# Kernel optimization log

Hardware: AMD Instinct MI355X
Metric: run time of the kernel (lower is better)

The kernel has to match this reference:

```python
import jax, jax.numpy as jnp
import numpy as np

B, N, D, H = 8, 2048, 128, 4
DH = D // H
EPS_LN = 1e-5


def setup_inputs() -> dict:
    key = jax.random.key(0)
    ks = jax.random.split(key, 9)
    x = jax.random.normal(ks[0], (B, N, D), dtype=jnp.float32)
    u = jax.random.uniform(ks[1], (N, N), dtype=jnp.float32)
    adj = jnp.where(u > 0.5, u, 0.0)
    adj = adj.at[jnp.arange(N), jnp.arange(N)].set(1.0)
    W = jax.random.normal(ks[2], (D, D), dtype=jnp.float32) * (1.0 / np.sqrt(D))
    a_src = jax.random.normal(ks[3], (H, DH), dtype=jnp.float32) * 0.02
    a_dst = jax.random.normal(ks[4], (H, DH), dtype=jnp.float32) * 0.02
    Wo = jax.random.normal(ks[5], (D, D), dtype=jnp.float32) * (1.0 / np.sqrt(D))
    bo = jnp.zeros((D,), dtype=jnp.float32)
    gamma = jnp.ones((D,), dtype=jnp.float32)
    beta = jnp.zeros((D,), dtype=jnp.float32)
    return {"x": x, "adj_static": adj, "W": W, "a_src": a_src, "a_dst": a_dst,
            "Wo": Wo, "bo": bo, "gamma": gamma, "beta": beta}


def reference(x, adj_static, W, a_src, a_dst, Wo, bo, gamma, beta):
    # h: (B, H, N, DH)
    h = (x @ W.T).reshape(B, N, H, DH).transpose(0, 2, 1, 3)
    src = jnp.einsum('bhnd,hd->bhn', h, a_src)  # (B, H, N)
    dst = jnp.einsum('bhnd,hd->bhn', h, a_dst)  # (B, H, N)
    e = jax.nn.leaky_relu(src[..., :, None] + dst[..., None, :], 0.2)  # (B,H,N,N)
    logA = jnp.log(jnp.clip(adj_static, 1e-8))[None, None]
    mask = (adj_static > 0)[None, None]
    e = jnp.where(mask, e + logA, -jnp.inf)
    attn = jax.nn.softmax(e, axis=-1)  # dropout is identity in eval mode
    out = attn @ h  # (B, H, N, DH)
    out = out.transpose(0, 2, 1, 3).reshape(B, N, D)
    out = out @ Wo.T + bo
    y = x + out
    mu = jnp.mean(y, axis=-1, keepdims=True)
    var = jnp.mean(jnp.square(y - mu), axis=-1, keepdims=True)
    return (y - mu) * jax.lax.rsqrt(var + EPS_LN) * gamma + beta
```

## Files before the change

### kernel.cpp

```cpp
#include <hip/hip_runtime.h>

typedef short bf16x8 __attribute__((ext_vector_type(8)));
typedef float f32x4  __attribute__((ext_vector_type(4)));
typedef float f32x2  __attribute__((ext_vector_type(2)));
typedef int   i32x4  __attribute__((ext_vector_type(4)));
typedef unsigned int u32x2 __attribute__((ext_vector_type(2)));

#define DEV static __device__ __forceinline__
#define LOG2E 1.4426950408889634f

DEV float bfu_to_f(unsigned short s) { return __builtin_bit_cast(float, (unsigned int)s << 16); }
DEV unsigned short f_to_bf(float f) {
  unsigned int u = __builtin_bit_cast(unsigned int, f);
  u += 0x7fffu + ((u >> 16) & 1u);
  return (unsigned short)(u >> 16);
}
DEV unsigned int pack_bf_rne(float lo, float hi) {
  return (unsigned int)f_to_bf(lo) | ((unsigned int)f_to_bf(hi) << 16);
}
DEV float nexp2(float x) {
#if __has_builtin(__builtin_amdgcn_exp2f)
  return __builtin_amdgcn_exp2f(x);
#else
  return exp2f(x);
#endif
}
template<bool HI> DEV unsigned int pk_fp8(float a, float b, unsigned int old) {
  return __builtin_amdgcn_cvt_pk_fp8_f32(a, b, old, HI);
}
template<int W> DEV f32x2 upk_fp8(unsigned int w) {
  auto r = __builtin_amdgcn_cvt_pk_f32_fp8(w, W);
  f32x2 o; o[0] = r[0]; o[1] = r[1]; return o;
}

DEV bool detect_f32(const void* adj) { return ((const float*)adj)[0] == 1.0f; }

template<bool F32> DEV float ldS(const void* p, size_t i) {
  if constexpr (F32) return ((const float*)p)[i];
  else               return bfu_to_f(((const unsigned short*)p)[i]);
}
template<bool F32> DEV void ld8f(const void* p, size_t i, float* o) {
  if constexpr (F32) {
    const float* f = (const float*)p + i;
    f32x4 a = *(const f32x4*)f, b = *(const f32x4*)(f + 4);
    o[0]=a[0]; o[1]=a[1]; o[2]=a[2]; o[3]=a[3];
    o[4]=b[0]; o[5]=b[1]; o[6]=b[2]; o[7]=b[3];
  } else {
    i32x4 w = *(const i32x4*)((const unsigned short*)p + i);
#pragma unroll
    for (int k = 0; k < 4; ++k) {
      unsigned int u = (unsigned int)w[k];
      o[2*k]   = __builtin_bit_cast(float, u << 16);
      o[2*k+1] = __builtin_bit_cast(float, u & 0xffff0000u);
    }
  }
}
template<bool F32> DEV bf16x8 ldfrag(const void* p, size_t i) {
  if constexpr (F32) {
    float o[8]; ld8f<true>(p, i, o);
    union { bf16x8 v; unsigned short u[8]; } r;
#pragma unroll
    for (int k = 0; k < 8; ++k) r.u[k] = f_to_bf(o[k]);
    return r.v;
  } else {
    return __builtin_bit_cast(bf16x8, *(const i32x4*)((const unsigned short*)p + i));
  }
}

__global__ __launch_bounds__(256) void k_prep(const void* __restrict__ adj,
                                              unsigned char* __restrict__ adjf) {
  const size_t i0 = ((size_t)blockIdx.x * 256 + threadIdx.x) * 8;
  u32x2 o;
  if (detect_f32(adj)) {
    const float* a = (const float*)adj + i0;
    f32x4 v0 = *(const f32x4*)a, v1 = *(const f32x4*)(a + 4);
    o[0] = pk_fp8<true>(v0[2], v0[3], pk_fp8<false>(v0[0], v0[1], 0u));
    o[1] = pk_fp8<true>(v1[2], v1[3], pk_fp8<false>(v1[0], v1[1], 0u));
  } else {
    i32x4 w = *(const i32x4*)((const unsigned short*)adj + i0);
    float f[8];
#pragma unroll
    for (int k = 0; k < 4; ++k) {
      unsigned int u = (unsigned int)w[k];
      f[2*k]   = __builtin_bit_cast(float, u << 16);
      f[2*k+1] = __builtin_bit_cast(float, u & 0xffff0000u);
    }
    o[0] = pk_fp8<true>(f[2], f[3], pk_fp8<false>(f[0], f[1], 0u));
    o[1] = pk_fp8<true>(f[6], f[7], pk_fp8<false>(f[4], f[5], 0u));
  }
  *(u32x2*)(adjf + i0) = o;
}

template<bool F32> DEV void k_h_body(const void* __restrict__ x, const void* __restrict__ W,
                                     unsigned char* __restrict__ hT,
                                     unsigned short (&t_s)[16][136]) {
  const int tid = threadIdx.x, lane = tid & 63, wave = tid >> 6;
  const int nt = blockIdx.x >> 3, ct = blockIdx.x & 7;
  const int m = lane & 15, q = lane >> 4;
  bf16x8 wf[4];
#pragma unroll
  for (int k = 0; k < 4; ++k)
    wf[k] = ldfrag<F32>(W, (size_t)(ct * 16 + m) * 128 + q * 8 + k * 32);
#pragma unroll
  for (int s = 0; s < 2; ++s) {
    const int nsub = wave * 2 + s;
    const size_t xr = (size_t)(nt * 128 + nsub * 16 + m) * 128 + q * 8;
    f32x4 acc = {0.f, 0.f, 0.f, 0.f};
#pragma unroll
    for (int k = 0; k < 4; ++k)
      acc = __builtin_amdgcn_mfma_f32_16x16x32_bf16(ldfrag<F32>(x, xr + k * 32), wf[k],
                                                    acc, 0, 0, 0);
    u32x2 w2; w2[0] = pack_bf_rne(acc[0], acc[1]); w2[1] = pack_bf_rne(acc[2], acc[3]);
    *(u32x2*)&t_s[m][nsub * 16 + q * 4] = w2;
  }
  __syncthreads();
  const int row = tid >> 4, c8 = tid & 15;
  const int chg = ct * 16 + row, hh = chg >> 5, dloc = chg & 31;
  const int ng = nt * 128 + c8 * 8, b = ng >> 11, nl = ng & 2047;
  i32x4 v = *(const i32x4*)&t_s[row][c8 * 8];
  float f[8];
#pragma unroll
  for (int k = 0; k < 4; ++k) {
    unsigned int u = (unsigned int)v[k];
    f[2*k]   = __builtin_bit_cast(float, u << 16);
    f[2*k+1] = __builtin_bit_cast(float, u & 0xffff0000u);
  }
  u32x2 o;
  o[0] = pk_fp8<true>(f[2], f[3], pk_fp8<false>(f[0], f[1], 0u));
  o[1] = pk_fp8<true>(f[6], f[7], pk_fp8<false>(f[4], f[5], 0u));
  *(u32x2*)(hT + ((size_t)((b * 4 + hh) * 32 + dloc)) * 2048 + nl) = o;
}
__global__ __launch_bounds__(256) void k_h(const void* x, const void* W,
                                           unsigned char* hT, const void* adj) {
  __shared__ __align__(16) unsigned short t_s[16][136];
  if (detect_f32(adj)) k_h_body<true>(x, W, hT, t_s); else k_h_body<false>(x, W, hT, t_s);
}

template<bool F32> DEV void k_sd_body(const unsigned char* __restrict__ hT,
                                      const void* __restrict__ a_src, const void* __restrict__ a_dst,
                                      float* __restrict__ rv, float* __restrict__ Fv,
                                      float* __restrict__ Hv) {
  const int t = blockIdx.x * 256 + threadIdx.x;
  const int n = t & 2047, bh = t >> 11, hh = bh & 3;
  const unsigned char* col = hT + (size_t)bh * 32 * 2048 + n;
  float s = 0.f, d = 0.f;
#pragma unroll
  for (int dd = 0; dd < 32; ++dd) {
    const float v = __builtin_amdgcn_cvt_f32_fp8((int)col[(size_t)dd * 2048], 0);
    s += v * ldS<F32>(a_src, hh * 32 + dd);
    d += v * ldS<F32>(a_dst, hh * 32 + dd);
  }
  rv[t] = nexp2(-0.8f * LOG2E * s);
  Fv[t] = nexp2(LOG2E * d);
  Hv[t] = nexp2(0.2f * LOG2E * d);
}
__global__ __launch_bounds__(256) void k_sd(const unsigned char* hT, const void* a_src,
                                            const void* a_dst, float* rv, float* Fv,
                                            float* Hv, const void* adj) {
  if (detect_f32(adj)) k_sd_body<true>(hT, a_src, a_dst, rv, Fv, Hv);
  else                 k_sd_body<false>(hT, a_src, a_dst, rv, Fv, Hv);
}

struct SmemAttn {
  unsigned char adj[2][64][144];
  unsigned char vt[2][32][144];
  float F[2][128];
  float H[2][128];
};

__global__ __launch_bounds__(512, 4) void k_attn(const unsigned char* __restrict__ adjf,
                                                 const unsigned char* __restrict__ hT,
                                                 const float* __restrict__ rv,
                                                 const float* __restrict__ Fv,
                                                 const float* __restrict__ Hv,
                                                 unsigned short* __restrict__ ao) {
  __shared__ __align__(16) SmemAttn sm;
  const int tid = threadIdx.x, lane = tid & 63, wave = tid >> 6;
  const int bh = blockIdx.x & 31, i64 = blockIdx.x >> 5;
  const int b = bh >> 2, hh = bh & 3;
  const int m = lane & 15, q = lane >> 4;
  const int i0 = i64 * 64;
  const int itile = wave >> 1, jh = wave & 1;
  const int il = itile * 16 + m;

  const int arow = tid >> 3, acol = (tid & 7) * 16;
  const int vd = tid >> 4, vcol = (tid & 15) * 8;
  const int scls = tid & 15;
  const bool dstg = scls < 2;
  const int dj = (tid >> 4) * 4;

  const unsigned char* ap = adjf + (size_t)(i0 + arow) * 2048 + acol;
  const unsigned char* vp = hT + ((size_t)bh * 32 + vd) * 2048 + vcol;
  const float* dp = (scls == 0 ? Fv : Hv) + (size_t)bh * 2048 + dj;
  float* dbase = (scls == 0 ? &sm.F[0][dj] : &sm.H[0][dj]);

  i32x4 ar; u32x2 vr; f32x4 dr;

  ar = *(const i32x4*)ap;
  vr = *(const u32x2*)vp;
  if (dstg) dr = *(const f32x4*)dp;
  *(i32x4*)&sm.adj[0][arow][acol] = ar;
  *(u32x2*)&sm.vt[0][vd][vcol] = vr;
  if (dstg) *(f32x4*)dbase = dr;
  __syncthreads();

  const float Ri = rv[bh * 2048 + i0 + il];
  const f32x2 Ri2 = {Ri, Ri};
  f32x4 acc0 = {0.f,0.f,0.f,0.f}, acc1 = {0.f,0.f,0.f,0.f};
  f32x4 acc2 = {0.f,0.f,0.f,0.f};
  const long Aones = 0x3838383838383838L;

  for (int c = 0; c < 16; ++c) {
    const int cb = c & 1;
    const bool pf = (c < 15);
    if (pf) {
      const int j1 = (c + 1) * 128;
      ar = *(const i32x4*)(ap + j1);
      vr = *(const u32x2*)(vp + j1);
      if (dstg) dr = *(const f32x4*)(dp + j1);
    }
#pragma unroll
    for (int jc = 0; jc < 2; ++jc) {
      const int jq = jh * 64 + jc * 32 + q * 8;
      u32x2 aw = *(const u32x2*)&sm.adj[cb][il][jq];
      f32x4 Fa = *(const f32x4*)&sm.F[cb][jq];
      f32x4 Fb = *(const f32x4*)&sm.F[cb][jq + 4];
      f32x4 Ha = *(const f32x4*)&sm.H[cb][jq];
      f32x4 Hb = *(const f32x4*)&sm.H[cb][jq + 4];
      long A0 = *(const long*)&sm.vt[cb][m][jq];
      long A1 = *(const long*)&sm.vt[cb][16 + m][jq];
      f32x2 av0 = upk_fp8<0>(aw[0]), av1 = upk_fp8<1>(aw[0]);
      f32x2 av2 = upk_fp8<0>(aw[1]), av3 = upk_fp8<1>(aw[1]);
      f32x2 f0 = {Fa[0],Fa[1]}, f1 = {Fa[2],Fa[3]};
      f32x2 f2 = {Fb[0],Fb[1]}, f3 = {Fb[2],Fb[3]};
      f32x2 h0 = {Ha[0],Ha[1]}, h1 = {Ha[2],Ha[3]};
      f32x2 h2 = {Hb[0],Hb[1]}, h3 = {Hb[2],Hb[3]};
      f32x2 w0 = __builtin_elementwise_max(f0, Ri2 * h0);
      f32x2 w1 = __builtin_elementwise_max(f1, Ri2 * h1);
      f32x2 w2 = __builtin_elementwise_max(f2, Ri2 * h2);
      f32x2 w3 = __builtin_elementwise_max(f3, Ri2 * h3);
      f32x2 pv0 = av0 * w0, pv1 = av1 * w1, pv2 = av2 * w2, pv3 = av3 * w3;
      u32x2 bp;
      bp[0] = pk_fp8<true>(pv1[0], pv1[1], pk_fp8<false>(pv0[0], pv0[1], 0u));
      bp[1] = pk_fp8<true>(pv3[0], pv3[1], pk_fp8<false>(pv2[0], pv2[1], 0u));
      const long B = __builtin_bit_cast(long, bp);
      acc0 = __builtin_amdgcn_mfma_f32_16x16x32_fp8_fp8(A0, B, acc0, 0, 0, 0);
      acc1 = __builtin_amdgcn_mfma_f32_16x16x32_fp8_fp8(A1, B, acc1, 0, 0, 0);
      acc2 = __builtin_amdgcn_mfma_f32_16x16x32_fp8_fp8(Aones, B, acc2, 0, 0, 0);
    }
    if (pf) {
      const int nb = cb ^ 1;
      *(i32x4*)&sm.adj[nb][arow][acol] = ar;
      *(u32x2*)&sm.vt[nb][vd][vcol] = vr;
      if (dstg) *(f32x4*)(dbase + nb * 128) = dr;
    }
    __syncthreads();
  }

  float* red = (float*)&sm;
  const int ridx = (itile * 64 + lane) * 12;
  if (jh == 1) {
    *(f32x4*)&red[ridx]     = acc0;
    *(f32x4*)&red[ridx + 4] = acc1;
    red[ridx + 8] = acc2[0];
  }
  __syncthreads();
  if (jh == 0) {
    acc0 += *(const f32x4*)&red[ridx];
    acc1 += *(const f32x4*)&red[ridx + 4];
    const float den = acc2[0] + red[ridx + 8];
    const float inv = 1.f / fmaxf(den, 1e-20f);
    unsigned short* op = ao + ((size_t)(b * 2048) + i0 + il) * 128 + hh * 32 + q * 4;
    u32x2 w0, w1;
    w0[0] = pack_bf_rne(acc0[0] * inv, acc0[1] * inv);
    w0[1] = pack_bf_rne(acc0[2] * inv, acc0[3] * inv);
    w1[0] = pack_bf_rne(acc1[0] * inv, acc1[1] * inv);
    w1[1] = pack_bf_rne(acc1[2] * inv, acc1[3] * inv);
    *(u32x2*)op        = w0;
    *(u32x2*)(op + 16) = w1;
  }
}

template<bool F32> DEV void k_out_body(const unsigned short* __restrict__ ao,
                                       const void* __restrict__ Wo, const void* __restrict__ bo,
                                       const void* __restrict__ x, const void* __restrict__ gamma,
                                       const void* __restrict__ beta, void* __restrict__ out,
                                       float (&y_s)[16][132]) {
  const int tid = threadIdx.x, lane = tid & 63, wave = tid >> 6;
  const int m = lane & 15, q = lane >> 4;
  const int rbase = blockIdx.x * 16;
  bf16x8 af[4];
#pragma unroll
  for (int k = 0; k < 4; ++k)
    af[k] = ldfrag<false>(ao, ((size_t)(rbase + m)) * 128 + q * 8 + k * 32);
  f32x4 acc[2] = {{0.f,0.f,0.f,0.f},{0.f,0.f,0.f,0.f}};
#pragma unroll
  for (int ct = 0; ct < 2; ++ct) {
    const size_t wrow = (size_t)(wave * 32 + ct * 16 + m) * 128 + q * 8;
#pragma unroll
    for (int k = 0; k < 4; ++k)
      acc[ct] = __builtin_amdgcn_mfma_f32_16x16x32_bf16(af[k], ldfrag<F32>(Wo, wrow + k * 32),
                                                        acc[ct], 0, 0, 0);
  }
#pragma unroll
  for (int ct = 0; ct < 2; ++ct) {
    const int c = wave * 32 + ct * 16 + m;
    const float bov = ldS<F32>(bo, c);
#pragma unroll
    for (int r = 0; r < 4; ++r) {
      const int row = q * 4 + r;
      y_s[row][c] = acc[ct][r] + bov + ldS<F32>(x, (size_t)(rbase + row) * 128 + c);
    }
  }
  __syncthreads();
  const int r = tid >> 4, c16 = tid & 15;
  float vals[8], sum = 0.f, sq = 0.f;
#pragma unroll
  for (int k = 0; k < 8; ++k) {
    const float v = y_s[r][c16 * 8 + k];
    vals[k] = v; sum += v; sq += v * v;
  }
#pragma unroll
  for (int msk = 1; msk < 16; msk <<= 1) {
    sum += __shfl_xor(sum, msk, 16);
    sq  += __shfl_xor(sq,  msk, 16);
  }
  const float mu  = sum * (1.f / 128.f);
  const float var = fmaxf(sq * (1.f / 128.f) - mu * mu, 0.f);
  const float rstd = rsqrtf(var + 1e-5f);
  float o[8];
#pragma unroll
  for (int k = 0; k < 8; ++k) {
    const int c = c16 * 8 + k;
    o[k] = (vals[k] - mu) * rstd * ldS<F32>(gamma, c) + ldS<F32>(beta, c);
  }
  const size_t obase = (size_t)(rbase + r) * 128 + c16 * 8;
  if constexpr (F32) {
    float* op = (float*)out + obase;
    f32x4 w0 = {o[0],o[1],o[2],o[3]}, w1 = {o[4],o[5],o[6],o[7]};
    *(f32x4*)op = w0; *(f32x4*)(op + 4) = w1;
  } else {
    union { unsigned short u[8]; i32x4 v; } ob;
#pragma unroll
    for (int k = 0; k < 8; ++k) ob.u[k] = f_to_bf(o[k]);
    *(i32x4*)((unsigned short*)out + obase) = ob.v;
  }
}
__global__ __launch_bounds__(256) void k_out(const unsigned short* ao, const void* Wo,
                                             const void* bo, const void* x, const void* gamma,
                                             const void* beta, void* out, const void* adj) {
  __shared__ __align__(16) float y_s[16][132];
  if (detect_f32(adj)) k_out_body<true>(ao, Wo, bo, x, gamma, beta, out, y_s);
  else                 k_out_body<false>(ao, Wo, bo, x, gamma, beta, out, y_s);
}

extern "C" void kernel_launch(void* const* d_in, const int* in_sizes, int n_in,
                              void* d_out, int out_size, void* d_ws, size_t ws_size,
                              hipStream_t stream) {
  const void* x     = d_in[0];
  const void* adj   = d_in[1];
  const void* W     = d_in[2];
  const void* a_src = d_in[3];
  const void* a_dst = d_in[4];
  const void* Wo    = d_in[5];
  const void* bo    = d_in[6];
  const void* gamma = d_in[7];
  const void* beta  = d_in[8];

  char* ws = (char*)d_ws;
  unsigned char*  hT_ws  = (unsigned char*)ws;
  unsigned short* ao_ws  = (unsigned short*)(ws + 2097152);
  float*          rv_ws  = (float*)(ws + 6291456);
  float*          Fv_ws  = (float*)(ws + 6553600);
  float*          Hv_ws  = (float*)(ws + 6815744);
  unsigned char*  adjf   = (unsigned char*)(ws + 7077888);

  k_prep<<<2048, 256, 0, stream>>>(adj, adjf);
  k_h   <<<1024, 256, 0, stream>>>(x, W, hT_ws, adj);
  k_sd  <<<256,  256, 0, stream>>>(hT_ws, a_src, a_dst, rv_ws, Fv_ws, Hv_ws, adj);
  k_attn<<<1024, 512, 0, stream>>>(adjf, hT_ws, rv_ws, Fv_ws, Hv_ws, ao_ws);
  k_out <<<1024, 256, 0, stream>>>(ao_ws, Wo, bo, x, gamma, beta, d_out, adj);
}
```

Measured before the change: 148.9 us.

## Drop LDS staging in attention; load operands directly into registers with bf16-packed F/H

The attention kernel no longer stages adjacency, value and F/H tiles through double-buffered shared memory with per-chunk barriers. Each wave now loads its own fragments straight from global memory into a two-deep register prefetch ring. F and H are stored as one packed bf16 pair per element, halving that traffic, and blocks shrink to 256 threads covering 32 rows, with twice as many blocks. This removes LDS round-trips and barriers, but operands shared across waves are now fetched redundantly from global/L2, and F/H lose precision to bf16.

```diff
diff --git a/kernel.cpp b/kernel.cpp
--- a/kernel.cpp
+++ b/kernel.cpp
@@ -18,6 +18,8 @@
 DEV unsigned int pack_bf_rne(float lo, float hi) {
   return (unsigned int)f_to_bf(lo) | ((unsigned int)f_to_bf(hi) << 16);
 }
+DEV float fplo(int u) { return __builtin_bit_cast(float, (unsigned int)u << 16); }
+DEV float fphi(int u) { return __builtin_bit_cast(float, (unsigned int)u & 0xffff0000u); }
 DEV float nexp2(float x) {
 #if __has_builtin(__builtin_amdgcn_exp2f)
   return __builtin_amdgcn_exp2f(x);
@@ -138,8 +140,7 @@
 
 template<bool F32> DEV void k_sd_body(const unsigned char* __restrict__ hT,
                                       const void* __restrict__ a_src, const void* __restrict__ a_dst,
-                                      float* __restrict__ rv, float* __restrict__ Fv,
-                                      float* __restrict__ Hv) {
+                                      float* __restrict__ rv, unsigned int* __restrict__ fhv) {
   const int t = blockIdx.x * 256 + threadIdx.x;
   const int n = t & 2047, bh = t >> 11, hh = bh & 3;
   const unsigned char* col = hT + (size_t)bh * 32 * 2048 + n;
@@ -151,113 +152,96 @@
     d += v * ldS<F32>(a_dst, hh * 32 + dd);
   }
   rv[t] = nexp2(-0.8f * LOG2E * s);
-  Fv[t] = nexp2(LOG2E * d);
-  Hv[t] = nexp2(0.2f * LOG2E * d);
+  const float F = nexp2(LOG2E * d);
+  const float H = nexp2(0.2f * LOG2E * d);
+  fhv[t] = pack_bf_rne(F, H);
 }
 __global__ __launch_bounds__(256) void k_sd(const unsigned char* hT, const void* a_src,
-                                            const void* a_dst, float* rv, float* Fv,
-                                            float* Hv, const void* adj) {
-  if (detect_f32(adj)) k_sd_body<true>(hT, a_src, a_dst, rv, Fv, Hv);
-  else                 k_sd_body<false>(hT, a_src, a_dst, rv, Fv, Hv);
-}
-
-struct SmemAttn {
-  unsigned char adj[2][64][144];
-  unsigned char vt[2][32][144];
-  float F[2][128];
-  float H[2][128];
+                                            const void* a_dst, float* rv, unsigned int* fhv,
+                                            const void* adj) {
+  if (detect_f32(adj)) k_sd_body<true>(hT, a_src, a_dst, rv, fhv);
+  else                 k_sd_body<false>(hT, a_src, a_dst, rv, fhv);
+}
+
+struct PrefRegs {
+  u32x2 aw[2];
+  long  a0[2], a1[2];
+  i32x4 fh0[2], fh1[2];
 };
 
-__global__ __launch_bounds__(512, 4) void k_attn(const unsigned char* __restrict__ adjf,
+DEV void pref_load(PrefRegs& r, const unsigned char* ap, const unsigned char* vp0,
+                   const unsigned char* vp1, const unsigned int* fp, int c) {
+#pragma unroll
+  for (int jc = 0; jc < 2; ++jc) {
+    const int off = c * 128 + jc * 32;
+    r.aw[jc]  = *(const u32x2*)(ap + off);
+    r.a0[jc]  = *(const long*)(vp0 + off);
+    r.a1[jc]  = *(const long*)(vp1 + off);
+    r.fh0[jc] = *(const i32x4*)(fp + off);
+    r.fh1[jc] = *(const i32x4*)(fp + off + 4);
+  }
+}
+
+DEV void attn_compute(const PrefRegs& r, const f32x2 Ri2,
+                      f32x4& acc0, f32x4& acc1, f32x4& acc2) {
+  const long Aones = 0x3838383838383838L;
+#pragma unroll
+  for (int jc = 0; jc < 2; ++jc) {
+    const u32x2 aw = r.aw[jc];
+    f32x2 av0 = upk_fp8<0>(aw[0]), av1 = upk_fp8<1>(aw[0]);
+    f32x2 av2 = upk_fp8<0>(aw[1]), av3 = upk_fp8<1>(aw[1]);
+    const i32x4 u0 = r.fh0[jc], u1 = r.fh1[jc];
+    f32x2 F0 = {fplo(u0[0]), fplo(u0[1])}, H0 = {fphi(u0[0]), fphi(u0[1])};
+    f32x2 F1 = {fplo(u0[2]), fplo(u0[3])}, H1 = {fphi(u0[2]), fphi(u0[3])};
+    f32x2 F2 = {fplo(u1[0]), fplo(u1[1])}, H2 = {fphi(u1[0]), fphi(u1[1])};
+    f32x2 F3 = {fplo(u1[2]), fplo(u1[3])}, H3 = {fphi(u1[2]), fphi(u1[3])};
+    f32x2 w0 = __builtin_elementwise_max(F0, Ri2 * H0);
+    f32x2 w1 = __builtin_elementwise_max(F1, Ri2 * H1);
+    f32x2 w2 = __builtin_elementwise_max(F2, Ri2 * H2);
+    f32x2 w3 = __builtin_elementwise_max(F3, Ri2 * H3);
+    f32x2 pv0 = av0 * w0, pv1 = av1 * w1, pv2 = av2 * w2, pv3 = av3 * w3;
+    u32x2 bp;
+    bp[0] = pk_fp8<true>(pv1[0], pv1[1], pk_fp8<false>(pv0[0], pv0[1], 0u));
+    bp[1] = pk_fp8<true>(pv3[0], pv3[1], pk_fp8<false>(pv2[0], pv2[1], 0u));
+    const long B = __builtin_bit_cast(long, bp);
+    acc0 = __builtin_amdgcn_mfma_f32_16x16x32_fp8_fp8(r.a0[jc], B, acc0, 0, 0, 0);
+    acc1 = __builtin_amdgcn_mfma_f32_16x16x32_fp8_fp8(r.a1[jc], B, acc1, 0, 0, 0);
+    acc2 = __builtin_amdgcn_mfma_f32_16x16x32_fp8_fp8(Aones,    B, acc2, 0, 0, 0);
+  }
+}
+
+__global__ __launch_bounds__(256, 4) void k_attn(const unsigned char* __restrict__ adjf,
                                                  const unsigned char* __restrict__ hT,
                                                  const float* __restrict__ rv,
-                                                 const float* __restrict__ Fv,
-                                                 const float* __restrict__ Hv,
+                                                 const unsigned int* __restrict__ fhv,
                                                  unsigned short* __restrict__ ao) {
-  __shared__ __align__(16) SmemAttn sm;
+  __shared__ __align__(16) float red[2 * 64 * 12];
   const int tid = threadIdx.x, lane = tid & 63, wave = tid >> 6;
-  const int bh = blockIdx.x & 31, i64 = blockIdx.x >> 5;
+  const int bh = blockIdx.x & 31, i32b = blockIdx.x >> 5;
   const int b = bh >> 2, hh = bh & 3;
   const int m = lane & 15, q = lane >> 4;
-  const int i0 = i64 * 64;
+  const int i0 = i32b * 32;
   const int itile = wave >> 1, jh = wave & 1;
   const int il = itile * 16 + m;
 
-  const int arow = tid >> 3, acol = (tid & 7) * 16;
-  const int vd = tid >> 4, vcol = (tid & 15) * 8;
-  const int scls = tid & 15;
-  const bool dstg = scls < 2;
-  const int dj = (tid >> 4) * 4;
-
-  const unsigned char* ap = adjf + (size_t)(i0 + arow) * 2048 + acol;
-  const unsigned char* vp = hT + ((size_t)bh * 32 + vd) * 2048 + vcol;
-  const float* dp = (scls == 0 ? Fv : Hv) + (size_t)bh * 2048 + dj;
-  float* dbase = (scls == 0 ? &sm.F[0][dj] : &sm.H[0][dj]);
-
-  i32x4 ar; u32x2 vr; f32x4 dr;
-
-  ar = *(const i32x4*)ap;
-  vr = *(const u32x2*)vp;
-  if (dstg) dr = *(const f32x4*)dp;
-  *(i32x4*)&sm.adj[0][arow][acol] = ar;
-  *(u32x2*)&sm.vt[0][vd][vcol] = vr;
-  if (dstg) *(f32x4*)dbase = dr;
-  __syncthreads();
+  const unsigned char* ap  = adjf + (size_t)(i0 + il) * 2048 + jh * 64 + q * 8;
+  const unsigned char* vp0 = hT + ((size_t)bh * 32 + m) * 2048 + jh * 64 + q * 8;
+  const unsigned char* vp1 = vp0 + 16 * 2048;
+  const unsigned int*  fp  = fhv + (size_t)bh * 2048 + jh * 64 + q * 8;
 
   const float Ri = rv[bh * 2048 + i0 + il];
   const f32x2 Ri2 = {Ri, Ri};
   f32x4 acc0 = {0.f,0.f,0.f,0.f}, acc1 = {0.f,0.f,0.f,0.f};
   f32x4 acc2 = {0.f,0.f,0.f,0.f};
-  const long Aones = 0x3838383838383838L;
-
+
+  PrefRegs r[2];
+  pref_load(r[0], ap, vp0, vp1, fp, 0);
+#pragma unroll
   for (int c = 0; c < 16; ++c) {
-    const int cb = c & 1;
-    const bool pf = (c < 15);
-    if (pf) {
-      const int j1 = (c + 1) * 128;
-      ar = *(const i32x4*)(ap + j1);
-      vr = *(const u32x2*)(vp + j1);
-      if (dstg) dr = *(const f32x4*)(dp + j1);
-    }
-#pragma unroll
-    for (int jc = 0; jc < 2; ++jc) {
-      const int jq = jh * 64 + jc * 32 + q * 8;
-      u32x2 aw = *(const u32x2*)&sm.adj[cb][il][jq];
-      f32x4 Fa = *(const f32x4*)&sm.F[cb][jq];
-      f32x4 Fb = *(const f32x4*)&sm.F[cb][jq + 4];
-      f32x4 Ha = *(const f32x4*)&sm.H[cb][jq];
-      f32x4 Hb = *(const f32x4*)&sm.H[cb][jq + 4];
-      long A0 = *(const long*)&sm.vt[cb][m][jq];
-      long A1 = *(const long*)&sm.vt[cb][16 + m][jq];
-      f32x2 av0 = upk_fp8<0>(aw[0]), av1 = upk_fp8<1>(aw[0]);
-      f32x2 av2 = upk_fp8<0>(aw[1]), av3 = upk_fp8<1>(aw[1]);
-      f32x2 f0 = {Fa[0],Fa[1]}, f1 = {Fa[2],Fa[3]};
-      f32x2 f2 = {Fb[0],Fb[1]}, f3 = {Fb[2],Fb[3]};
-      f32x2 h0 = {Ha[0],Ha[1]}, h1 = {Ha[2],Ha[3]};
-      f32x2 h2 = {Hb[0],Hb[1]}, h3 = {Hb[2],Hb[3]};
-      f32x2 w0 = __builtin_elementwise_max(f0, Ri2 * h0);
-      f32x2 w1 = __builtin_elementwise_max(f1, Ri2 * h1);
-      f32x2 w2 = __builtin_elementwise_max(f2, Ri2 * h2);
-      f32x2 w3 = __builtin_elementwise_max(f3, Ri2 * h3);
-      f32x2 pv0 = av0 * w0, pv1 = av1 * w1, pv2 = av2 * w2, pv3 = av3 * w3;
-      u32x2 bp;
-      bp[0] = pk_fp8<true>(pv1[0], pv1[1], pk_fp8<false>(pv0[0], pv0[1], 0u));
-      bp[1] = pk_fp8<true>(pv3[0], pv3[1], pk_fp8<false>(pv2[0], pv2[1], 0u));
-      const long B = __builtin_bit_cast(long, bp);
-      acc0 = __builtin_amdgcn_mfma_f32_16x16x32_fp8_fp8(A0, B, acc0, 0, 0, 0);
-      acc1 = __builtin_amdgcn_mfma_f32_16x16x32_fp8_fp8(A1, B, acc1, 0, 0, 0);
-      acc2 = __builtin_amdgcn_mfma_f32_16x16x32_fp8_fp8(Aones, B, acc2, 0, 0, 0);
-    }
-    if (pf) {
-      const int nb = cb ^ 1;
-      *(i32x4*)&sm.adj[nb][arow][acol] = ar;
-      *(u32x2*)&sm.vt[nb][vd][vcol] = vr;
-      if (dstg) *(f32x4*)(dbase + nb * 128) = dr;
-    }
-    __syncthreads();
-  }
-
-  float* red = (float*)&sm;
+    if (c < 15) pref_load(r[(c + 1) & 1], ap, vp0, vp1, fp, c + 1);
+    attn_compute(r[c & 1], Ri2, acc0, acc1, acc2);
+  }
+
   const int ridx = (itile * 64 + lane) * 12;
   if (jh == 1) {
     *(f32x4*)&red[ridx]     = acc0;
@@ -371,13 +355,12 @@
   unsigned char*  hT_ws  = (unsigned char*)ws;
   unsigned short* ao_ws  = (unsigned short*)(ws + 2097152);
   float*          rv_ws  = (float*)(ws + 6291456);
-  float*          Fv_ws  = (float*)(ws + 6553600);
-  float*          Hv_ws  = (float*)(ws + 6815744);
-  unsigned char*  adjf   = (unsigned char*)(ws + 7077888);
+  unsigned int*   fh_ws  = (unsigned int*)(ws + 6553600);
+  unsigned char*  adjf   = (unsigned char*)(ws + 6815744);
 
   k_prep<<<2048, 256, 0, stream>>>(adj, adjf);
   k_h   <<<1024, 256, 0, stream>>>(x, W, hT_ws, adj);
-  k_sd  <<<256,  256, 0, stream>>>(hT_ws, a_src, a_dst, rv_ws, Fv_ws, Hv_ws, adj);
-  k_attn<<<1024, 512, 0, stream>>>(adjf, hT_ws, rv_ws, Fv_ws, Hv_ws, ao_ws);
+  k_sd  <<<256,  256, 0, stream>>>(hT_ws, a_src, a_dst, rv_ws, fh_ws, adj);
+  k_attn<<<2048, 256, 0, stream>>>(adjf, hT_ws, rv_ws, fh_ws, ao_ws);
   k_out <<<1024, 256, 0, stream>>>(ao_ws, Wo, bo, x, gamma, beta, d_out, adj);
 }
```

New measurement: 218.0 us. +46.4%, slower.
